# Optimization experiments

Measured on AMD Instinct MI355X. Metric: run time of the kernel, lower is better.

The kernel has to match this reference:

```python
import jax, jax.numpy as jnp
import numpy as np

D_MODEL, N_HEADS, D_FF = 1024, 16, 4096
SCALE = 0.1          # lookup-activation input quantization step
NUM_BITS = 8
LEVELS = 1 << NUM_BITS   # 256
HALF = LEVELS // 2       # 128
MAX_EXP = 4
EPS = 1e-5


def pow2_weight(key, shape, max_exp=MAX_EXP):
    """Ternary power-of-two weights: values in {0, +/-2^{-e}}, e in [max_exp, max_exp+3].
    Exponent range keeps fan-in-1024 outputs O(1)."""
    k1, k2 = jax.random.split(key)
    sign = jax.random.randint(k1, shape, -1, 2).astype(jnp.float32)  # {-1,0,1}
    e = jax.random.randint(k2, shape, max_exp, max_exp + 4).astype(jnp.float32)
    return sign * jnp.exp2(-e)


def setup_inputs() -> dict:
    key = jax.random.key(0)
    ks = jax.random.split(key, 8)
    x = jax.random.normal(ks[0], (4, 2048, D_MODEL), dtype=jnp.float32)
    return {
        "x": x,
        "ln1_g": jnp.ones((D_MODEL,), jnp.float32),
        "ln1_b": jnp.zeros((D_MODEL,), jnp.float32),
        "wq": pow2_weight(ks[1], (D_MODEL, D_MODEL)),
        "wk": pow2_weight(ks[2], (D_MODEL, D_MODEL)),
        "wv": pow2_weight(ks[3], (D_MODEL, D_MODEL)),
        "wo": pow2_weight(ks[4], (D_MODEL, D_MODEL)),
        "ln2_g": jnp.ones((D_MODEL,), jnp.float32),
        "ln2_b": jnp.zeros((D_MODEL,), jnp.float32),
        "w1": pow2_weight(ks[5], (D_MODEL, D_FF)),
        "w2": pow2_weight(ks[6], (D_FF, D_MODEL)),
    }


def _layernorm(x, g, b):
    mu = jnp.mean(x, axis=-1, keepdims=True)
    var = jnp.var(x, axis=-1, keepdims=True)
    return (x - mu) * jax.lax.rsqrt(var + EPS) * g + b


def _lookup_act(x):
    # StructuredLookupActivation: quantize input to 2^num_bits levels, gather from
    # a precomputed GELU table (proved via Lasso lookup in the SNARK).
    grid = (jnp.arange(LEVELS, dtype=jnp.float32) - HALF) * SCALE
    table = jax.nn.gelu(grid)
    idx = jnp.clip(jnp.round(x / SCALE).astype(jnp.int32) + HALF, 0, LEVELS - 1)
    return table[idx]


def _linear_attention(x, wq, wk, wv, wo):
    B, S, D = x.shape
    H, Dh = N_HEADS, D // N_HEADS
    q = (x @ wq).reshape(B, S, H, Dh)
    k = (x @ wk).reshape(B, S, H, Dh)
    v = (x @ wv).reshape(B, S, H, Dh)
    # elu+1 feature map -> O(S*Dh^2) linear attention (no [S,S] scores)
    phi_q = jax.nn.elu(q) + 1.0
    phi_k = jax.nn.elu(k) + 1.0
    kv = jnp.einsum('bshd,bshe->bhde', phi_k, v)          # [B,H,Dh,Dh]
    z = jnp.sum(phi_k, axis=1)                            # [B,H,Dh]
    num = jnp.einsum('bshd,bhde->bshe', phi_q, kv)        # [B,S,H,Dh]
    den = jnp.einsum('bshd,bhd->bsh', phi_q, z)[..., None] + 1e-6
    out = (num / den).reshape(B, S, D)
    return out @ wo


def reference(x, ln1_g, ln1_b, wq, wk, wv, wo, ln2_g, ln2_b, w1, w2):
    # norm -> linear attention -> residual
    x = x + _linear_attention(_layernorm(x, ln1_g, ln1_b), wq, wk, wv, wo)
    # norm -> ternary FFN with lookup activation -> residual
    h = _layernorm(x, ln2_g, ln2_b)
    x = x + (_lookup_act(h @ w1) @ w2)
    return x
```

## Files before the change

kernel.cpp:

```cpp
#include <hip/hip_runtime.h>
#include <cstdint>
#include <cstddef>


#define D_MODEL 1024
#define SEQ     2048
#define BATCH   4
#define NTOK    8192
#define NHEADS  16
#define DH      64
#define DFF     4096
#define KVCH    16
#define CHROWS  (SEQ / KVCH)
#define PSTRIDE 4160

typedef _Float16 half8 __attribute__((ext_vector_type(8)));
typedef float f32x4 __attribute__((ext_vector_type(4)));

__device__ __forceinline__ unsigned short f2h(float x) {
  _Float16 h = (_Float16)x;
  union { _Float16 h; unsigned short u; } c; c.h = h; return c.u;
}
__device__ __forceinline__ float h2f(unsigned short u) {
  union { unsigned short u; _Float16 h; } c; c.u = u; return (float)c.h;
}

__device__ __forceinline__ float phi_act(float x) {
  return x > 0.f ? x + 1.f : expf(x);
}

__device__ __forceinline__ float gelu_exact(float v) {
  float c = 0.7978845608028654f;
  float t = tanhf(c * (v + 0.044715f * v * v * v));
  return 0.5f * v * (1.f + t);
}

__device__ __forceinline__ void gl_lds16(const void* g, void* l) {
  __builtin_amdgcn_global_load_lds(
      (const __attribute__((address_space(1))) unsigned int*)g,
      (__attribute__((address_space(3))) unsigned int*)l, 16, 0, 0);
}

__global__ __launch_bounds__(256) void convT(const float* __restrict__ W,
                                             unsigned short* __restrict__ WT,
                                             int K, int N) {
  __shared__ float tile[64][65];
  int kb = blockIdx.y << 6, nb = blockIdx.x << 6;
  int t = threadIdx.x;
  int rr = t >> 4, cc = (t & 15) << 2;
#pragma unroll
  for (int i = 0; i < 4; ++i) {
    int r = rr + (i << 4);
    float4 v = *(const float4*)(W + (size_t)(kb + r) * N + nb + cc);
    tile[r][cc] = v.x; tile[r][cc + 1] = v.y; tile[r][cc + 2] = v.z; tile[r][cc + 3] = v.w;
  }
  __syncthreads();
#pragma unroll
  for (int i = 0; i < 4; ++i) {
    int n = rr + (i << 4);
    ushort4 o;
    o.x = f2h(tile[cc + 0][n]); o.y = f2h(tile[cc + 1][n]);
    o.z = f2h(tile[cc + 2][n]); o.w = f2h(tile[cc + 3][n]);
    *(ushort4*)(WT + (size_t)(nb + n) * K + kb + cc) = o;
  }
}

__global__ __launch_bounds__(256) void ln_kernel(const float* __restrict__ X,
                                                 const float* __restrict__ g,
                                                 const float* __restrict__ b,
                                                 unsigned short* __restrict__ Y) {
  int tok = blockIdx.x;
  int t = threadIdx.x;
  const float4* xr = (const float4*)(X + (size_t)tok * D_MODEL);
  float4 v = xr[t];
  float s  = v.x + v.y + v.z + v.w;
  float s2 = v.x * v.x + v.y * v.y + v.z * v.z + v.w * v.w;
#pragma unroll
  for (int o = 32; o > 0; o >>= 1) {
    s  += __shfl_down(s, o);
    s2 += __shfl_down(s2, o);
  }
  __shared__ float red[8];
  __shared__ float mu_s, rs_s;
  int wid = t >> 6;
  if ((t & 63) == 0) { red[wid] = s; red[wid + 4] = s2; }
  __syncthreads();
  if (t == 0) {
    float ts  = red[0] + red[1] + red[2] + red[3];
    float ts2 = red[4] + red[5] + red[6] + red[7];
    float mu  = ts * (1.f / D_MODEL);
    float var = ts2 * (1.f / D_MODEL) - mu * mu;
    mu_s = mu;
    rs_s = rsqrtf(var + 1e-5f);
  }
  __syncthreads();
  float mu = mu_s, rs = rs_s;
  float4 gv = ((const float4*)g)[t];
  float4 bv = ((const float4*)b)[t];
  ushort4 hv;
  hv.x = f2h((v.x - mu) * rs * gv.x + bv.x);
  hv.y = f2h((v.y - mu) * rs * gv.y + bv.y);
  hv.z = f2h((v.z - mu) * rs * gv.z + bv.z);
  hv.w = f2h((v.w - mu) * rs * gv.w + bv.w);
  ((ushort4*)(Y + (size_t)tok * D_MODEL))[t] = hv;
}

template <int EP, int BK>
__global__ __launch_bounds__(256, (BK == 64) ? 4 : 2) void mfma_gemm(
    const unsigned short* __restrict__ A,
    const unsigned short* __restrict__ BT,
    void* Cv, const float* R, int N, int K) {
  constexpr int SEGS = BK / 8;
  constexpr int RPC  = 64 / SEGS;
  constexpr int NJ   = 32 / RPC;
  __shared__ unsigned short smem[2 * 128 * BK];
  __shared__ float gtab[EP == 3 ? 256 : 1];
  unsigned short* sA = smem;
  unsigned short* sB = smem + 128 * BK;

  int t = threadIdx.x;
  if (EP == 3) gtab[t & 255] = gelu_exact((float)((t & 255) - 128) * 0.1f);

  int bm, bn;
  {
    int L = blockIdx.y * gridDim.x + blockIdx.x;
    if ((gridDim.y & 7) == 0) {
      int xcd = L & 7, wi = L >> 3;
      int mPerX = gridDim.y >> 3;
      bm = xcd * mPerX + wi / gridDim.x;
      bn = wi % gridDim.x;
    } else {
      bn = blockIdx.x; bm = blockIdx.y;
    }
  }

  int w = t >> 6, l = t & 63;
  int lrow = l / SEGS;
  int lseg = l & (SEGS - 1);
  int m0 = bm << 7;
  int n0 = bn << 7;
  size_t strideB = (size_t)K * 2;

  const char* gA[NJ]; const char* gB[NJ];
  int ldsOff[NJ];
#pragma unroll
  for (int j = 0; j < NJ; ++j) {
    int row = (w << 5) + j * RPC + lrow;
    int gso = (lseg ^ (row & 7)) << 4;
    gA[j] = (const char*)A + (size_t)(m0 + row) * strideB + gso;
    gB[j] = (const char*)BT + (size_t)(n0 + row) * strideB + gso;
    ldsOff[j] = ((w << 5) + j * RPC) * BK;
  }

  int wm = w >> 1, wn = w & 1;
  int m16 = l & 15, qd = l >> 4;

  f32x4 acc[4][4];
#pragma unroll
  for (int i = 0; i < 4; ++i)
#pragma unroll
    for (int j = 0; j < 4; ++j) acc[i][j] = (f32x4){0.f, 0.f, 0.f, 0.f};

  for (int k0 = 0; k0 < K; k0 += BK) {
    size_t kb = (size_t)k0 * 2;
#pragma unroll
    for (int j = 0; j < NJ; ++j) {
      gl_lds16(gA[j] + kb, sA + ldsOff[j]);
      gl_lds16(gB[j] + kb, sB + ldsOff[j]);
    }
    __syncthreads();
#pragma unroll
    for (int kk = 0; kk < BK / 32; ++kk) {
      int ksb = (kk << 2) + qd;
      half8 af[4], bf[4];
#pragma unroll
      for (int mt = 0; mt < 4; ++mt) {
        int r = (wm << 6) + (mt << 4) + m16;
        int slot = ksb ^ (r & 7);
        af[mt] = *(const half8*)(sA + r * BK + (slot << 3));
      }
#pragma unroll
      for (int nt = 0; nt < 4; ++nt) {
        int r = (wn << 6) + (nt << 4) + m16;
        int slot = ksb ^ (r & 7);
        bf[nt] = *(const half8*)(sB + r * BK + (slot << 3));
      }
#pragma unroll
      for (int mt = 0; mt < 4; ++mt)
#pragma unroll
        for (int nt = 0; nt < 4; ++nt)
          acc[mt][nt] = __builtin_amdgcn_mfma_f32_16x16x32_f16(af[mt], bf[nt], acc[mt][nt], 0, 0, 0);
    }
    __syncthreads();
  }

  int sel = n0 >> 10;
  size_t slab = (size_t)sel * ((size_t)NTOK * D_MODEL);
  int colL = (n0 & 1023) + (wn << 6) + m16;

  int colBase = n0 + (wn << 6) + m16;
#pragma unroll
  for (int mt = 0; mt < 4; ++mt) {
    int rBase = m0 + (wm << 6) + (mt << 4) + (qd << 2);
#pragma unroll
    for (int nt = 0; nt < 4; ++nt) {
      int col = colBase + (nt << 4);
#pragma unroll
      for (int i = 0; i < 4; ++i) {
        float v = acc[mt][nt][i];
        if (EP == 4) {
          if (sel < 2) v = phi_act(v);
          size_t idx = slab + (size_t)(rBase + i) * D_MODEL + colL + (nt << 4);
          ((unsigned short*)Cv)[idx] = f2h(v);
        } else {
          size_t idx = (size_t)(rBase + i) * N + col;
          if (EP == 2)      ((float*)Cv)[idx] = R[idx] + v;
          else if (EP == 3) {
            float r = rintf(v / 0.1f);
            int iq = (int)r + 128;
            iq = iq < 0 ? 0 : (iq > 255 ? 255 : iq);
            ((unsigned short*)Cv)[idx] = f2h(gtab[iq]);
          } else          ((float*)Cv)[idx] = v;
        }
      }
    }
  }
}

template <int EP>
__global__ __launch_bounds__(512, 2) void gemm8p(
    const unsigned short* __restrict__ A,
    const unsigned short* __restrict__ BT,
    void* Cv, int N, int K) {
  __shared__ unsigned short smem[65536];
  __shared__ float gtab[EP == 3 ? 256 : 1];
  char* sm = (char*)smem;

  int t = threadIdx.x;
  if (EP == 3) gtab[t & 255] = gelu_exact((float)((t & 255) - 128) * 0.1f);

  int bm, bn;
  {
    int L = blockIdx.y * gridDim.x + blockIdx.x;
    if ((gridDim.y & 7) == 0) {
      int xcd = L & 7, wi = L >> 3;
      int mPerX = gridDim.y >> 3;
      bm = xcd * mPerX + wi / gridDim.x;
      bn = wi % gridDim.x;
    } else {
      bn = blockIdx.x; bm = blockIdx.y;
    }
  }
  int m0 = bm << 8, n0 = bn << 8;

  int w = t >> 6, l = t & 63;
  int wm = w >> 2, wn = w & 3;
  int m16 = l & 15, qd = l >> 4;

  const int aBase = wm * 8 * 2048 + (l << 4);
  const int bBase = 65536 + wn * 4 * 2048 + (l << 4);

  const char* gAs[2]; const char* gBs[2]; int ldsg[2];
#pragma unroll
  for (int i = 0; i < 2; ++i) {
    int g = 2 * w + i;
    gAs[i] = (const char*)A  + ((size_t)(m0 + g * 16 + m16) * K + qd * 8) * 2;
    gBs[i] = (const char*)BT + ((size_t)(n0 + g * 16 + m16) * K + qd * 8) * 2;
    ldsg[i] = g * 2048;
  }

#define STG(GP, D, KK, KB) do {                                           \
    int _b = ((GP) ? 65536 : 0) + (D) * 32768 + (KK) * 1024;              \
    size_t _ko = (size_t)((KB) + (KK) * 32) * 2;                          \
    const char* _g0 = (GP) ? gBs[0] : gAs[0];                             \
    const char* _g1 = (GP) ? gBs[1] : gAs[1];                             \
    gl_lds16(_g0 + _ko, sm + _b + ldsg[0]);                               \
    gl_lds16(_g1 + _ko, sm + _b + ldsg[1]);                               \
  } while (0)

  f32x4 acc[8][4];
#pragma unroll
  for (int i = 0; i < 8; ++i)
#pragma unroll
    for (int j = 0; j < 4; ++j) acc[i][j] = (f32x4){0.f, 0.f, 0.f, 0.f};

  STG(0, 0, 0, 0); STG(1, 0, 0, 0); STG(0, 0, 1, 0); STG(1, 0, 1, 0);
  asm volatile("s_waitcnt vmcnt(4)" ::: "memory");
  __builtin_amdgcn_s_barrier();

  half8 af[4], bf[4];
  int NT = K >> 6;

#define PHASE(KKv, MB, RELOADB, SGP, SKK, VM) do {                         \
    const char* _pa = sm + curb + aBase + (MB) * 2048 + (KKv) * 1024;      \
    _Pragma("unroll")                                                      \
    for (int mt = 0; mt < 4; ++mt)                                         \
      af[mt] = *(const half8*)(_pa + mt * 2048);                           \
    if (RELOADB) {                                                         \
      const char* _pb = sm + curb + bBase + (KKv) * 1024;                  \
      _Pragma("unroll")                                                    \
      for (int nt = 0; nt < 4; ++nt)                                       \
        bf[nt] = *(const half8*)(_pb + nt * 2048);                         \
    }                                                                      \
    STG(SGP, nxt, SKK, k0n);                                               \
    __builtin_amdgcn_s_barrier();                                          \
    asm volatile("s_waitcnt lgkmcnt(0)" ::: "memory");                     \
    __builtin_amdgcn_sched_barrier(0);                                     \
    __builtin_amdgcn_s_setprio(1);                                         \
    _Pragma("unroll")                                                      \
    for (int mt = 0; mt < 4; ++mt)                                         \
      _Pragma("unroll")                                                    \
      for (int nt = 0; nt < 4; ++nt)                                       \
        acc[mt + (MB)][nt] = __builtin_amdgcn_mfma_f32_16x16x32_f16(       \
            af[mt], bf[nt], acc[mt + (MB)][nt], 0, 0, 0);                  \
    __builtin_amdgcn_s_setprio(0);                                         \
    if (VM) asm volatile("s_waitcnt vmcnt(4)" ::: "memory");               \
    __builtin_amdgcn_s_barrier();                                          \
  } while (0)

  for (int tt = 0; tt < NT; ++tt) {
    int cur = tt & 1, nxt = cur ^ 1;
    int k0n = (tt + 1 < NT) ? ((tt + 1) << 6) : 0;
    int curb = cur * 32768;

    PHASE(0, 0, 1, 0, 0, 0);
    PHASE(0, 4, 0, 1, 0, 1);
    PHASE(1, 0, 1, 0, 1, 0);
    PHASE(1, 4, 0, 1, 1, 1);
  }
#undef PHASE
#undef STG

  int sel = n0 >> 10;
  size_t slab = (size_t)sel * ((size_t)NTOK * D_MODEL);
  int colBase = n0 + (wn << 6) + m16;
#pragma unroll
  for (int mt = 0; mt < 8; ++mt) {
    int rBase = m0 + wm * 128 + (mt << 4) + (qd << 2);
#pragma unroll
    for (int nt = 0; nt < 4; ++nt) {
      int col = colBase + (nt << 4);
#pragma unroll
      for (int i = 0; i < 4; ++i) {
        float v = acc[mt][nt][i];
        if (EP == 4) {
          if (sel < 2) v = phi_act(v);
          size_t idx = slab + (size_t)(rBase + i) * D_MODEL + (col & 1023);
          ((unsigned short*)Cv)[idx] = f2h(v);
        } else {
          float r = rintf(v / 0.1f);
          int iq = (int)r + 128;
          iq = iq < 0 ? 0 : (iq > 255 ? 255 : iq);
          ((unsigned short*)Cv)[(size_t)(rBase + i) * N + col] = f2h(gtab[iq]);
        }
      }
    }
  }
}

__global__ __launch_bounds__(256) void kvz_partial(const unsigned short* __restrict__ PK,
                                                   const unsigned short* __restrict__ V,
                                                   float* __restrict__ P) {
  int c = blockIdx.x, bh = blockIdx.y;
  int b = bh >> 4, h = bh & 15;
  __shared__ float pk[8][64];
  __shared__ float vv[8][64];
  int t = threadIdx.x;
  const size_t base = ((size_t)b * SEQ + (size_t)c * CHROWS) * D_MODEL + h * DH;
  int u = t & 127;
  int lrow = u >> 4;
  int lcol = (u & 15) << 2;
  bool isV = (t >= 128);
  const unsigned short* src = isV ? V : PK;
  int dkb = (t >> 4) << 2;
  int deb = (t & 15) << 2;
  float acc[4][4] = {};
  float zacc = 0.f;
  for (int s0 = 0; s0 < CHROWS; s0 += 8) {
    ushort4 ld = *(const ushort4*)(src + base + (size_t)(s0 + lrow) * D_MODEL + lcol);
    float f0 = h2f(ld.x), f1 = h2f(ld.y), f2 = h2f(ld.z), f3 = h2f(ld.w);
    __syncthreads();
    if (isV) { vv[lrow][lcol] = f0; vv[lrow][lcol+1] = f1; vv[lrow][lcol+2] = f2; vv[lrow][lcol+3] = f3; }
    else     { pk[lrow][lcol] = f0; pk[lrow][lcol+1] = f1; pk[lrow][lcol+2] = f2; pk[lrow][lcol+3] = f3; }
    __syncthreads();
#pragma unroll
    for (int ss = 0; ss < 8; ++ss) {
      float4 a  = *(const float4*)&pk[ss][dkb];
      float4 bb = *(const float4*)&vv[ss][deb];
      acc[0][0] += a.x * bb.x; acc[0][1] += a.x * bb.y; acc[0][2] += a.x * bb.z; acc[0][3] += a.x * bb.w;
      acc[1][0] += a.y * bb.x; acc[1][1] += a.y * bb.y; acc[1][2] += a.y * bb.z; acc[1][3] += a.y * bb.w;
      acc[2][0] += a.z * bb.x; acc[2][1] += a.z * bb.y; acc[2][2] += a.z * bb.z; acc[2][3] += a.z * bb.w;
      acc[3][0] += a.w * bb.x; acc[3][1] += a.w * bb.y; acc[3][2] += a.w * bb.z; acc[3][3] += a.w * bb.w;
    }
    if (t < 64) {
#pragma unroll
      for (int ss = 0; ss < 8; ++ss) zacc += pk[ss][t];
    }
  }
  float* Pb = P + ((size_t)c * 64 + bh) * PSTRIDE;
#pragma unroll
  for (int i = 0; i < 4; ++i) {
    float4 o; o.x = acc[i][0]; o.y = acc[i][1]; o.z = acc[i][2]; o.w = acc[i][3];
    *(float4*)(Pb + (size_t)(dkb + i) * DH + deb) = o;
  }
  if (t < 64) Pb[4096 + t] = zacc;
}

__global__ __launch_bounds__(256) void kvz_reduce(const float* __restrict__ P,
                                                  float* __restrict__ KV,
                                                  float* __restrict__ Z) {
  int bh = blockIdx.x;
  int t = threadIdx.x;
  for (int i = t; i < PSTRIDE; i += 256) {
    float s = 0.f;
#pragma unroll
    for (int c = 0; c < KVCH; ++c)
      s += P[((size_t)c * 64 + bh) * PSTRIDE + i];
    if (i < 4096) KV[(size_t)bh * 4096 + i] = s;
    else          Z[(size_t)bh * 64 + (i - 4096)] = s;
  }
}

__global__ __launch_bounds__(256) void attn_kernel(const unsigned short* __restrict__ PQ,
                                                   const float* __restrict__ KVm,
                                                   const float* __restrict__ Z,
                                                   unsigned short* __restrict__ O) {
  int s0 = blockIdx.x << 6;
  int h = blockIdx.y, b = blockIdx.z;
  __shared__ float Pqt[64][64];
  __shared__ float Kv[64][64];
  __shared__ float den[64];
  __shared__ float zsh[64];
  int t = threadIdx.x;
  size_t qbase  = ((size_t)b * SEQ + s0) * D_MODEL + h * DH;
  size_t kvbase = (size_t)(b * NHEADS + h) * (DH * DH);
  int r0 = t >> 4;
  int c4 = (t & 15) << 2;
#pragma unroll
  for (int rr = 0; rr < 4; ++rr) {
    int row = r0 + (rr << 4);
    *(float4*)&Kv[row][c4] = *(const float4*)(KVm + kvbase + (size_t)row * DH + c4);
    ushort4 q = *(const ushort4*)(PQ + qbase + (size_t)row * D_MODEL + c4);
    Pqt[c4 + 0][row] = h2f(q.x);
    Pqt[c4 + 1][row] = h2f(q.y);
    Pqt[c4 + 2][row] = h2f(q.z);
    Pqt[c4 + 3][row] = h2f(q.w);
  }
  if (t < 16) *(float4*)&zsh[t << 2] = *(const float4*)(Z + (size_t)(b * NHEADS + h) * DH + (t << 2));
  __syncthreads();
  if (t < 64) {
    float d_ = 1e-6f;
#pragma unroll
    for (int dd = 0; dd < 64; ++dd) d_ += Pqt[dd][t] * zsh[dd];
    den[t] = d_;
  }
  __syncthreads();
  int tokb = (t >> 4) << 2, eb = (t & 15) << 2;
  float acc[4][4] = {};
#pragma unroll 8
  for (int dd = 0; dd < 64; ++dd) {
    float4 a  = *(const float4*)&Pqt[dd][tokb];
    float4 bb = *(const float4*)&Kv[dd][eb];
    acc[0][0] += a.x * bb.x; acc[0][1] += a.x * bb.y; acc[0][2] += a.x * bb.z; acc[0][3] += a.x * bb.w;
    acc[1][0] += a.y * bb.x; acc[1][1] += a.y * bb.y; acc[1][2] += a.y * bb.z; acc[1][3] += a.y * bb.w;
    acc[2][0] += a.z * bb.x; acc[2][1] += a.z * bb.y; acc[2][2] += a.z * bb.z; acc[2][3] += a.z * bb.w;
    acc[3][0] += a.w * bb.x; acc[3][1] += a.w * bb.y; acc[3][2] += a.w * bb.z; acc[3][3] += a.w * bb.w;
  }
#pragma unroll
  for (int i = 0; i < 4; ++i) {
    float dv = den[tokb + i];
    ushort4 hv;
    hv.x = f2h(acc[i][0] / dv);
    hv.y = f2h(acc[i][1] / dv);
    hv.z = f2h(acc[i][2] / dv);
    hv.w = f2h(acc[i][3] / dv);
    size_t oidx = ((size_t)b * SEQ + s0 + tokb + i) * D_MODEL + h * DH + eb;
    *(ushort4*)(O + oidx) = hv;
  }
}

extern "C" void kernel_launch(void* const* d_in, const int* in_sizes, int n_in,
                              void* d_out, int out_size, void* d_ws, size_t ws_size,
                              hipStream_t stream) {
  const float* x    = (const float*)d_in[0];
  const float* ln1g = (const float*)d_in[1];
  const float* ln1b = (const float*)d_in[2];
  const float* wq   = (const float*)d_in[3];
  const float* wk   = (const float*)d_in[4];
  const float* wv   = (const float*)d_in[5];
  const float* wo   = (const float*)d_in[6];
  const float* ln2g = (const float*)d_in[7];
  const float* ln2b = (const float*)d_in[8];
  const float* w1   = (const float*)d_in[9];
  const float* w2   = (const float*)d_in[10];
  float* out = (float*)d_out;
  char* ws = (char*)d_ws;

  const size_t MB = 1024 * 1024;
  unsigned short* xn   = (unsigned short*)(ws);
  unsigned short* qkv  = (unsigned short*)(ws + 32 * MB);
  unsigned short* phiq = qkv;
  unsigned short* phik = qkv + (size_t)NTOK * D_MODEL;
  unsigned short* vbuf = qkv + 2 * (size_t)NTOK * D_MODEL;
  unsigned short* ffn  = (unsigned short*)(ws + 32 * MB);
  unsigned short* w1T  = (unsigned short*)(ws + 96 * MB);
  unsigned short* w2T  = (unsigned short*)(ws + 104 * MB);
  unsigned short* woT  = (unsigned short*)(ws + 128 * MB);

  unsigned short* wqkvT = (unsigned short*)d_out;
  float* kvP = (float*)((char*)d_out + 6 * MB);
  float* kv  = (float*)((char*)d_out + 24 * MB);
  float* z   = (float*)((char*)d_out + 25 * MB);

  dim3 blk(256);
  dim3 blk8(512);
  dim3 gcD(D_MODEL / 64, D_MODEL / 64);

  convT<<<gcD, blk, 0, stream>>>(wq, wqkvT, D_MODEL, D_MODEL);
  convT<<<gcD, blk, 0, stream>>>(wk, wqkvT + (size_t)D_MODEL * D_MODEL, D_MODEL, D_MODEL);
  convT<<<gcD, blk, 0, stream>>>(wv, wqkvT + 2 * (size_t)D_MODEL * D_MODEL, D_MODEL, D_MODEL);
  convT<<<gcD, blk, 0, stream>>>(wo, woT, D_MODEL, D_MODEL);

  ln_kernel<<<NTOK, blk, 0, stream>>>(x, ln1g, ln1b, xn);

  dim3 gQKV(3 * D_MODEL / 256, NTOK / 256);
  gemm8p<4><<<gQKV, blk8, 0, stream>>>(xn, wqkvT, qkv, 3 * D_MODEL, D_MODEL);

  kvz_partial<<<dim3(KVCH, BATCH * NHEADS), blk, 0, stream>>>(phik, vbuf, kvP);
  kvz_reduce<<<BATCH * NHEADS, blk, 0, stream>>>(kvP, kv, z);

  attn_kernel<<<dim3(SEQ / 64, NHEADS, BATCH), blk, 0, stream>>>(phiq, kv, z, xn);

  convT<<<dim3(DFF / 64, D_MODEL / 64), blk, 0, stream>>>(w1, w1T, D_MODEL, DFF);
  convT<<<dim3(D_MODEL / 64, DFF / 64), blk, 0, stream>>>(w2, w2T, DFF, D_MODEL);

  dim3 gD(D_MODEL / 128, NTOK / 128);
  mfma_gemm<2, 128><<<gD, blk, 0, stream>>>(xn, woT, out, x, D_MODEL, D_MODEL);

  ln_kernel<<<NTOK, blk, 0, stream>>>(out, ln2g, ln2b, xn);

  dim3 gF(DFF / 256, NTOK / 256);
  gemm8p<3><<<gF, blk8, 0, stream>>>(xn, w1T, ffn, DFF, D_MODEL);

  mfma_gemm<2, 128><<<gD, blk, 0, stream>>>(ffn, w2T, out, out, D_MODEL, DFF);
}
```

Baseline: 496.2 us.

## Replace direct global-to-LDS loads with register-staged prefetch and fewer barriers

The GEMM main loop stops using direct global-to-LDS async loads (gl_lds16) and instead prefetches the next K tile into registers during the MFMA phases, writing it to the other LDS buffer later in the iteration. Per-phase barriers drop from eight per iteration to one, and the A fragments for the second M half are held in a separate register set. The aim is less synchronisation stall and better overlap of global loads with MFMA work. The cost is more VGPRs for staging, which may lower occupancy, plus extra LDS write instructions. Global-load latency is also exposed if one iteration of compute is not enough to hide it.

```diff
diff --git a/kernel.cpp b/kernel.cpp
--- a/kernel.cpp
+++ b/kernel.cpp
@@ -16,6 +16,7 @@
 
 typedef _Float16 half8 __attribute__((ext_vector_type(8)));
 typedef float f32x4 __attribute__((ext_vector_type(4)));
+typedef unsigned int u32x4 __attribute__((ext_vector_type(4)));
 
 __device__ __forceinline__ unsigned short f2h(float x) {
   _Float16 h = (_Float16)x;
@@ -256,27 +257,17 @@
   int w = t >> 6, l = t & 63;
   int wm = w >> 2, wn = w & 3;
   int m16 = l & 15, qd = l >> 4;
-
-  const int aBase = wm * 8 * 2048 + (l << 4);
-  const int bBase = 65536 + wn * 4 * 2048 + (l << 4);
-
-  const char* gAs[2]; const char* gBs[2]; int ldsg[2];
-#pragma unroll
-  for (int i = 0; i < 2; ++i) {
-    int g = 2 * w + i;
-    gAs[i] = (const char*)A  + ((size_t)(m0 + g * 16 + m16) * K + qd * 8) * 2;
-    gBs[i] = (const char*)BT + ((size_t)(n0 + g * 16 + m16) * K + qd * 8) * 2;
-    ldsg[i] = g * 2048;
-  }
-
-#define STG(GP, D, KK, KB) do {                                           \
-    int _b = ((GP) ? 65536 : 0) + (D) * 32768 + (KK) * 1024;              \
-    size_t _ko = (size_t)((KB) + (KK) * 32) * 2;                          \
-    const char* _g0 = (GP) ? gBs[0] : gAs[0];                             \
-    const char* _g1 = (GP) ? gBs[1] : gAs[1];                             \
-    gl_lds16(_g0 + _ko, sm + _b + ldsg[0]);                               \
-    gl_lds16(_g1 + _ko, sm + _b + ldsg[1]);                               \
-  } while (0)
+  int lw = l << 4;
+
+  const int aBase = wm * 8 * 2048 + lw;
+  const int bBase = 65536 + wn * 4 * 2048 + lw;
+
+  const char* gA0 = (const char*)A  + ((size_t)(m0 + (2 * w) * 16 + m16) * K + qd * 8) * 2;
+  const char* gA1 = (const char*)A  + ((size_t)(m0 + (2 * w + 1) * 16 + m16) * K + qd * 8) * 2;
+  const char* gB0 = (const char*)BT + ((size_t)(n0 + (2 * w) * 16 + m16) * K + qd * 8) * 2;
+  const char* gB1 = (const char*)BT + ((size_t)(n0 + (2 * w + 1) * 16 + m16) * K + qd * 8) * 2;
+  const int wrg0 = (2 * w) * 2048 + lw;
+  const int wrg1 = (2 * w + 1) * 2048 + lw;
 
   f32x4 acc[8][4];
 #pragma unroll
@@ -284,52 +275,110 @@
 #pragma unroll
     for (int j = 0; j < 4; ++j) acc[i][j] = (f32x4){0.f, 0.f, 0.f, 0.f};
 
-  STG(0, 0, 0, 0); STG(1, 0, 0, 0); STG(0, 0, 1, 0); STG(1, 0, 1, 0);
-  asm volatile("s_waitcnt vmcnt(4)" ::: "memory");
+  half8 af[4], af2[4], bf[4];
+  u32x4 sA0, sA1, sA2, sA3, sB0, sB1, sB2, sB3;
+
+  sA0 = *(const u32x4*)(gA0);       sA1 = *(const u32x4*)(gA1);
+  sA2 = *(const u32x4*)(gA0 + 64);  sA3 = *(const u32x4*)(gA1 + 64);
+  sB0 = *(const u32x4*)(gB0);       sB1 = *(const u32x4*)(gB1);
+  sB2 = *(const u32x4*)(gB0 + 64);  sB3 = *(const u32x4*)(gB1 + 64);
+  *(u32x4*)(sm + wrg0)                 = sA0;
+  *(u32x4*)(sm + wrg1)                 = sA1;
+  *(u32x4*)(sm + wrg0 + 1024)          = sA2;
+  *(u32x4*)(sm + wrg1 + 1024)          = sA3;
+  *(u32x4*)(sm + 65536 + wrg0)         = sB0;
+  *(u32x4*)(sm + 65536 + wrg1)         = sB1;
+  *(u32x4*)(sm + 65536 + wrg0 + 1024)  = sB2;
+  *(u32x4*)(sm + 65536 + wrg1 + 1024)  = sB3;
+  asm volatile("s_waitcnt lgkmcnt(0)" ::: "memory");
   __builtin_amdgcn_s_barrier();
 
-  half8 af[4], bf[4];
-  int NT = K >> 6;
-
-#define PHASE(KKv, MB, RELOADB, SGP, SKK, VM) do {                         \
-    const char* _pa = sm + curb + aBase + (MB) * 2048 + (KKv) * 1024;      \
-    _Pragma("unroll")                                                      \
-    for (int mt = 0; mt < 4; ++mt)                                         \
-      af[mt] = *(const half8*)(_pa + mt * 2048);                           \
-    if (RELOADB) {                                                         \
-      const char* _pb = sm + curb + bBase + (KKv) * 1024;                  \
-      _Pragma("unroll")                                                    \
-      for (int nt = 0; nt < 4; ++nt)                                       \
-        bf[nt] = *(const half8*)(_pb + nt * 2048);                         \
-    }                                                                      \
-    STG(SGP, nxt, SKK, k0n);                                               \
-    __builtin_amdgcn_s_barrier();                                          \
-    asm volatile("s_waitcnt lgkmcnt(0)" ::: "memory");                     \
-    __builtin_amdgcn_sched_barrier(0);                                     \
-    __builtin_amdgcn_s_setprio(1);                                         \
-    _Pragma("unroll")                                                      \
-    for (int mt = 0; mt < 4; ++mt)                                         \
-      _Pragma("unroll")                                                    \
-      for (int nt = 0; nt < 4; ++nt)                                       \
-        acc[mt + (MB)][nt] = __builtin_amdgcn_mfma_f32_16x16x32_f16(       \
-            af[mt], bf[nt], acc[mt + (MB)][nt], 0, 0, 0);                  \
-    __builtin_amdgcn_s_setprio(0);                                         \
-    if (VM) asm volatile("s_waitcnt vmcnt(4)" ::: "memory");               \
-    __builtin_amdgcn_s_barrier();                                          \
-  } while (0)
-
+  const int NT = K >> 6;
   for (int tt = 0; tt < NT; ++tt) {
-    int cur = tt & 1, nxt = cur ^ 1;
-    int k0n = (tt + 1 < NT) ? ((tt + 1) << 6) : 0;
-    int curb = cur * 32768;
-
-    PHASE(0, 0, 1, 0, 0, 0);
-    PHASE(0, 4, 0, 1, 0, 1);
-    PHASE(1, 0, 1, 0, 1, 0);
-    PHASE(1, 4, 0, 1, 1, 1);
-  }
-#undef PHASE
-#undef STG
+    const int curb = (tt & 1) * 32768;
+    const int nxtb = curb ^ 32768;
+    const size_t kn = (size_t)((tt + 1 < NT) ? ((tt + 1) << 6) : 0) * 2;
+    const char* pa = sm + curb + aBase;
+    const char* pb = sm + curb + bBase;
+
+    af[0] = *(const half8*)(pa);
+    af[1] = *(const half8*)(pa + 2048);
+    af[2] = *(const half8*)(pa + 4096);
+    af[3] = *(const half8*)(pa + 6144);
+    bf[0] = *(const half8*)(pb);
+    bf[1] = *(const half8*)(pb + 2048);
+    bf[2] = *(const half8*)(pb + 4096);
+    bf[3] = *(const half8*)(pb + 6144);
+    sA0 = *(const u32x4*)(gA0 + kn);
+    sA1 = *(const u32x4*)(gA1 + kn);
+    sA2 = *(const u32x4*)(gA0 + kn + 64);
+    sA3 = *(const u32x4*)(gA1 + kn + 64);
+    __builtin_amdgcn_s_setprio(1);
+#pragma unroll
+    for (int mt = 0; mt < 4; ++mt)
+#pragma unroll
+      for (int nt = 0; nt < 4; ++nt)
+        acc[mt][nt] = __builtin_amdgcn_mfma_f32_16x16x32_f16(af[mt], bf[nt], acc[mt][nt], 0, 0, 0);
+    __builtin_amdgcn_s_setprio(0);
+    __builtin_amdgcn_sched_barrier(0);
+
+    af2[0] = *(const half8*)(pa + 8192);
+    af2[1] = *(const half8*)(pa + 10240);
+    af2[2] = *(const half8*)(pa + 12288);
+    af2[3] = *(const half8*)(pa + 14336);
+    sB0 = *(const u32x4*)(gB0 + kn);
+    sB1 = *(const u32x4*)(gB1 + kn);
+    sB2 = *(const u32x4*)(gB0 + kn + 64);
+    sB3 = *(const u32x4*)(gB1 + kn + 64);
+    __builtin_amdgcn_s_setprio(1);
+#pragma unroll
+    for (int mt = 0; mt < 4; ++mt)
+#pragma unroll
+      for (int nt = 0; nt < 4; ++nt)
+        acc[mt + 4][nt] = __builtin_amdgcn_mfma_f32_16x16x32_f16(af2[mt], bf[nt], acc[mt + 4][nt], 0, 0, 0);
+    __builtin_amdgcn_s_setprio(0);
+    __builtin_amdgcn_sched_barrier(0);
+
+    af[0] = *(const half8*)(pa + 1024);
+    af[1] = *(const half8*)(pa + 1024 + 2048);
+    af[2] = *(const half8*)(pa + 1024 + 4096);
+    af[3] = *(const half8*)(pa + 1024 + 6144);
+    bf[0] = *(const half8*)(pb + 1024);
+    bf[1] = *(const half8*)(pb + 1024 + 2048);
+    bf[2] = *(const half8*)(pb + 1024 + 4096);
+    bf[3] = *(const half8*)(pb + 1024 + 6144);
+    *(u32x4*)(sm + nxtb + wrg0)        = sA0;
+    *(u32x4*)(sm + nxtb + wrg1)        = sA1;
+    *(u32x4*)(sm + nxtb + wrg0 + 1024) = sA2;
+    *(u32x4*)(sm + nxtb + wrg1 + 1024) = sA3;
+    __builtin_amdgcn_s_setprio(1);
+#pragma unroll
+    for (int mt = 0; mt < 4; ++mt)
+#pragma unroll
+      for (int nt = 0; nt < 4; ++nt)
+        acc[mt][nt] = __builtin_amdgcn_mfma_f32_16x16x32_f16(af[mt], bf[nt], acc[mt][nt], 0, 0, 0);
+    __builtin_amdgcn_s_setprio(0);
+    __builtin_amdgcn_sched_barrier(0);
+
+    af2[0] = *(const half8*)(pa + 1024 + 8192);
+    af2[1] = *(const half8*)(pa + 1024 + 10240);
+    af2[2] = *(const half8*)(pa + 1024 + 12288);
+    af2[3] = *(const half8*)(pa + 1024 + 14336);
+    *(u32x4*)(sm + nxtb + 65536 + wrg0)        = sB0;
+    *(u32x4*)(sm + nxtb + 65536 + wrg1)        = sB1;
+    *(u32x4*)(sm + nxtb + 65536 + wrg0 + 1024) = sB2;
+    *(u32x4*)(sm + nxtb + 65536 + wrg1 + 1024) = sB3;
+    __builtin_amdgcn_s_setprio(1);
+#pragma unroll
+    for (int mt = 0; mt < 4; ++mt)
+#pragma unroll
+      for (int nt = 0; nt < 4; ++nt)
+        acc[mt + 4][nt] = __builtin_amdgcn_mfma_f32_16x16x32_f16(af2[mt], bf[nt], acc[mt + 4][nt], 0, 0, 0);
+    __builtin_amdgcn_s_setprio(0);
+    asm volatile("s_waitcnt lgkmcnt(0)" ::: "memory");
+    __builtin_amdgcn_sched_barrier(0);
+    __builtin_amdgcn_s_barrier();
+  }
 
   int sel = n0 >> 10;
   size_t slab = (size_t)sel * ((size_t)NTOK * D_MODEL);
```

After: 517.0 us. 4.2% more time.
